# Kernel tuning notes

Measured on AMD Instinct MI355X. Metric: run time of the kernel, lower is better.

The kernel has to match this reference:

```python
import jax, jax.numpy as jnp
import numpy as np

N = 2048
D_MODEL = 1024
N_HEADS = 16
D_HEAD = D_MODEL // N_HEADS


def setup_inputs() -> dict:
    key = jax.random.key(0)
    ks = jax.random.split(key, 12)
    s = 1.0 / np.sqrt(D_MODEL)
    inp = {
        "x": jax.random.normal(ks[0], (N, D_MODEL), dtype=jnp.float32),
        "edge_bias": jax.random.normal(ks[1], (N, N, N_HEADS), dtype=jnp.float32) * 0.1,
        # torch.nn.Linear convention: y = x @ W.T + b, W: [out, in]
        "Wq": jax.random.normal(ks[2], (D_MODEL, D_MODEL), dtype=jnp.float32) * s,
        "bq": jax.random.normal(ks[3], (D_MODEL,), dtype=jnp.float32) * s,
        "Wk": jax.random.normal(ks[4], (D_MODEL, D_MODEL), dtype=jnp.float32) * s,
        "bk": jax.random.normal(ks[5], (D_MODEL,), dtype=jnp.float32) * s,
        "Wv": jax.random.normal(ks[6], (D_MODEL, D_MODEL), dtype=jnp.float32) * s,
        "bv": jax.random.normal(ks[7], (D_MODEL,), dtype=jnp.float32) * s,
        "Wo": jax.random.normal(ks[8], (D_MODEL, D_MODEL), dtype=jnp.float32) * s,
        "bo": jax.random.normal(ks[9], (D_MODEL,), dtype=jnp.float32) * s,
    }
    return inp


def reference(x, edge_bias, Wq, bq, Wk, bk, Wv, bv, Wo, bo):
    # x: [N, d], edge_bias: [N, N, H]
    scale = D_HEAD ** -0.5
    q = (x @ Wq.T + bq).reshape(N, N_HEADS, D_HEAD)  # [N, H, Dh]
    k = (x @ Wk.T + bk).reshape(N, N_HEADS, D_HEAD)
    v = (x @ Wv.T + bv).reshape(N, N_HEADS, D_HEAD)
    # attn[h, i, j] = q_i . k_j * scale + edge_bias[i, j, h]
    attn = jnp.einsum("nhd,mhd->hnm", q, k) * scale
    attn = attn + jnp.transpose(edge_bias, (2, 0, 1))
    attn = jax.nn.softmax(attn, axis=-1)
    # dropout is identity in eval/reference mode
    out = jnp.einsum("hnm,mhd->nhd", attn, v).reshape(N, D_MODEL)
    return out @ Wo.T + bo
```

## Files before the change

### kernel.cpp

```cpp
#include <hip/hip_runtime.h>
#include <math.h>

#define NTOK 2048
#define DM   1024
#define NH   16
#define DH   64
#define GM   2048
#define GN   1024
#define GK   1024
#define SCALE 0.125f

typedef __attribute__((ext_vector_type(8))) short short8;
typedef __attribute__((ext_vector_type(4))) float floatx4;
typedef unsigned short ushort_t;

__device__ __forceinline__ unsigned short f2bf(float f) {
    unsigned u = __builtin_bit_cast(unsigned, f);
    u += 0x7fffu + ((u >> 16) & 1u);
    return (unsigned short)(u >> 16);
}

__global__ __launch_bounds__(256) void convert5(
    const float* __restrict__ x,  const float* __restrict__ wq,
    const float* __restrict__ wk, const float* __restrict__ wv,
    const float* __restrict__ wo, ushort_t* __restrict__ dst)
{
    const size_t i4 = (size_t)blockIdx.x * 256 + threadIdx.x;
    const float* src; size_t off;
    if      (i4 <  524288) { src = x;  off = 0;       }
    else if (i4 <  786432) { src = wq; off = 524288;  }
    else if (i4 < 1048576) { src = wk; off = 786432;  }
    else if (i4 < 1310720) { src = wv; off = 1048576; }
    else                   { src = wo; off = 1310720; }
    float4 v = ((const float4*)src)[i4 - off];
    ushort4 o;
    o.x = f2bf(v.x); o.y = f2bf(v.y); o.z = f2bf(v.z); o.w = f2bf(v.w);
    ((ushort4*)dst)[i4] = o;
}

template<int BM, int BN>
__global__ __launch_bounds__(256) void gemm_bt(
    const ushort_t* __restrict__ A,
    const ushort_t* __restrict__ B0, const ushort_t* __restrict__ B1,
    const ushort_t* __restrict__ B2,
    const float* __restrict__ bi0, const float* __restrict__ bi1,
    const float* __restrict__ bi2,
    void* C0, void* C1, void* C2, int mode0, int mode1, int mode2)
{
    constexpr int AC = BM * 4 / 256;
    constexpr int BC = BN * 4 / 256;
    constexpr int FI = BM / 32;
    constexpr int FJ = BN / 32;
    constexpr int WM = BM / 2;
    constexpr int WN = BN / 2;

    const int z = blockIdx.z;
    const ushort_t* B   = (z == 0) ? B0  : (z == 1) ? B1  : B2;
    const float*    bia = (z == 0) ? bi0 : (z == 1) ? bi1 : bi2;
    void*           C   = (z == 0) ? C0  : (z == 1) ? C1  : C2;
    const int mode      = (z == 0) ? mode0 : (z == 1) ? mode1 : mode2;

    __shared__ __align__(16) ushort_t As[BM][32];
    __shared__ __align__(16) ushort_t Bs[BN][32];

    const int t    = threadIdx.x;
    const int w    = t >> 6;
    const int L    = t & 63;
    const int r16  = L & 15;
    const int quad = L >> 4;
    const int wm   = w & 1;
    const int wn   = w >> 1;

    const int m0 = blockIdx.y * BM;
    const int n0 = blockIdx.x * BN;

    const int srow = t >> 2;
    const int skc  = (t & 3) * 8;

    const ushort_t* ap = A + (size_t)(m0 + srow) * GK + skc;
    const ushort_t* bp = B + (size_t)(n0 + srow) * GK + skc;

    floatx4 acc[FI][FJ];
#pragma unroll
    for (int i = 0; i < FI; ++i)
#pragma unroll
        for (int j = 0; j < FJ; ++j) acc[i][j] = (floatx4){0.f, 0.f, 0.f, 0.f};

    short8 areg[AC], breg[BC];
#pragma unroll
    for (int c = 0; c < AC; ++c) areg[c] = *(const short8*)(ap + (size_t)c * 64 * GK);
#pragma unroll
    for (int c = 0; c < BC; ++c) breg[c] = *(const short8*)(bp + (size_t)c * 64 * GK);

    for (int ks = 0; ks < GK / 32; ++ks) {
        __syncthreads();
#pragma unroll
        for (int c = 0; c < AC; ++c) *(short8*)&As[c * 64 + srow][skc] = areg[c];
#pragma unroll
        for (int c = 0; c < BC; ++c) *(short8*)&Bs[c * 64 + srow][skc] = breg[c];
        __syncthreads();
        if (ks < GK / 32 - 1) {
            ap += 32; bp += 32;
#pragma unroll
            for (int c = 0; c < AC; ++c) areg[c] = *(const short8*)(ap + (size_t)c * 64 * GK);
#pragma unroll
            for (int c = 0; c < BC; ++c) breg[c] = *(const short8*)(bp + (size_t)c * 64 * GK);
        }
        short8 af[FI], bf[FJ];
#pragma unroll
        for (int fi = 0; fi < FI; ++fi)
            af[fi] = *(const short8*)&As[wm * WM + fi * 16 + r16][quad * 8];
#pragma unroll
        for (int fj = 0; fj < FJ; ++fj)
            bf[fj] = *(const short8*)&Bs[wn * WN + fj * 16 + r16][quad * 8];
#pragma unroll
        for (int fi = 0; fi < FI; ++fi)
#pragma unroll
            for (int fj = 0; fj < FJ; ++fj)
                acc[fi][fj] = __builtin_amdgcn_mfma_f32_16x16x32_bf16(
                    af[fi], bf[fj], acc[fi][fj], 0, 0, 0);
    }

#pragma unroll
    for (int fj = 0; fj < FJ; ++fj) {
        const int col = n0 + wn * WN + fj * 16 + r16;
        const float bv = bia[col];
#pragma unroll
        for (int fi = 0; fi < FI; ++fi) {
            const int row0 = m0 + wm * WM + fi * 16 + 4 * quad;
            floatx4 c = acc[fi][fj];
            if (mode == 2) {
                float* Cf = (float*)C;
#pragma unroll
                for (int i = 0; i < 4; ++i)
                    Cf[(size_t)(row0 + i) * GN + col] = c[i] + bv;
            } else if (mode == 0) {
                ushort_t* Cb = (ushort_t*)C;
#pragma unroll
                for (int i = 0; i < 4; ++i)
                    Cb[(size_t)(row0 + i) * GN + col] = f2bf(c[i] + bv);
            } else {
                ushort_t* Cb = (ushort_t*)C;
                ushort4 pk;
                pk.x = f2bf(c[0] + bv); pk.y = f2bf(c[1] + bv);
                pk.z = f2bf(c[2] + bv); pk.w = f2bf(c[3] + bv);
                *(ushort4*)(Cb + (size_t)col * GM + row0) = pk;
            }
        }
    }
}

#define NT (NTOK / 32)

__global__ __launch_bounds__(256) void attn2(
    const ushort_t* __restrict__ q, const ushort_t* __restrict__ k,
    const ushort_t* __restrict__ vT, const float* __restrict__ bias,
    ushort_t* __restrict__ ao)
{
    __shared__ float    Bb[2][4][16][33];
    __shared__ ushort_t Ps[4][16][40];

    const int b    = blockIdx.x;
    const int hg   = (b >> 3) & 3;
    const int it   = (b & 7) | ((b >> 5) << 3);
    const int i0   = it * 16;
    const int t    = threadIdx.x;
    const int w    = t >> 6;
    const int L    = t & 63;
    const int r16  = L & 15;
    const int quad = L >> 4;
    const int h    = hg * 4 + w;

#define kAddr(J0, JH, KC) (k  + (size_t)((J0) + (JH)*16 + r16) * DM + h*DH + (KC)*32 + quad*8)
#define vAddr(J0, DB)     (vT + (size_t)(h*DH + (DB)*16 + r16) * NTOK + (J0) + quad*8)
#define bAddr(J0, CI)     (bias + ((size_t)(i0 + (CI)*8 + (t>>5)) * NTOK + (J0) + (t&31)) * NH + hg*4)

    short8 qf[2];
#pragma unroll
    for (int kc = 0; kc < 2; ++kc)
        qf[kc] = *(const short8*)(q + (size_t)(i0 + r16) * DM + h * DH + kc * 32 + quad * 8);

    short8 kf[2][4];
    short8 vf[2][4];
    float4 bst[2];

    kf[0][0] = *(const short8*)kAddr(0, 0, 0);
    kf[0][1] = *(const short8*)kAddr(0, 0, 1);
    kf[0][2] = *(const short8*)kAddr(0, 1, 0);
    kf[0][3] = *(const short8*)kAddr(0, 1, 1);
    vf[0][0] = *(const short8*)vAddr(0, 0);
    vf[0][1] = *(const short8*)vAddr(0, 1);
    vf[0][2] = *(const short8*)vAddr(0, 2);
    vf[0][3] = *(const short8*)vAddr(0, 3);
    bst[0] = *(const float4*)bAddr(0, 0);
    bst[1] = *(const float4*)bAddr(0, 1);
    Bb[0][0][0 + (t >> 5)][t & 31] = bst[0].x;
    Bb[0][1][0 + (t >> 5)][t & 31] = bst[0].y;
    Bb[0][2][0 + (t >> 5)][t & 31] = bst[0].z;
    Bb[0][3][0 + (t >> 5)][t & 31] = bst[0].w;
    Bb[0][0][8 + (t >> 5)][t & 31] = bst[1].x;
    Bb[0][1][8 + (t >> 5)][t & 31] = bst[1].y;
    Bb[0][2][8 + (t >> 5)][t & 31] = bst[1].z;
    Bb[0][3][8 + (t >> 5)][t & 31] = bst[1].w;
    __syncthreads();

    floatx4 o[4];
#pragma unroll
    for (int d = 0; d < 4; ++d) o[d] = (floatx4){0.f, 0.f, 0.f, 0.f};
    float lrow[4] = {0.f, 0.f, 0.f, 0.f};

#define TILE(JT, CUR, NXT)                                                      \
  {                                                                             \
    const bool pre = (JT) < NT - 1;                                             \
    const int j0n = ((JT) + 1) * 32;                                            \
    if (pre) {                                                                  \
      kf[NXT][0] = *(const short8*)kAddr(j0n, 0, 0);                            \
      kf[NXT][1] = *(const short8*)kAddr(j0n, 0, 1);                            \
      kf[NXT][2] = *(const short8*)kAddr(j0n, 1, 0);                            \
      kf[NXT][3] = *(const short8*)kAddr(j0n, 1, 1);                            \
      vf[NXT][0] = *(const short8*)vAddr(j0n, 0);                               \
      vf[NXT][1] = *(const short8*)vAddr(j0n, 1);                               \
      vf[NXT][2] = *(const short8*)vAddr(j0n, 2);                               \
      vf[NXT][3] = *(const short8*)vAddr(j0n, 3);                               \
      bst[0] = *(const float4*)bAddr(j0n, 0);                                   \
      bst[1] = *(const float4*)bAddr(j0n, 1);                                   \
    }                                                                           \
    floatx4 s0 = (floatx4){0.f, 0.f, 0.f, 0.f};                                 \
    floatx4 s1 = (floatx4){0.f, 0.f, 0.f, 0.f};                                 \
    s0 = __builtin_amdgcn_mfma_f32_16x16x32_bf16(qf[0], kf[CUR][0], s0, 0,0,0); \
    s0 = __builtin_amdgcn_mfma_f32_16x16x32_bf16(qf[1], kf[CUR][1], s0, 0,0,0); \
    s1 = __builtin_amdgcn_mfma_f32_16x16x32_bf16(qf[0], kf[CUR][2], s1, 0,0,0); \
    s1 = __builtin_amdgcn_mfma_f32_16x16x32_bf16(qf[1], kf[CUR][3], s1, 0,0,0); \
    _Pragma("unroll")                                                           \
    for (int ii = 0; ii < 4; ++ii) {                                            \
      const float bv0 = Bb[CUR][w][4 * quad + ii][r16];                         \
      const float bv1 = Bb[CUR][w][4 * quad + ii][16 + r16];                    \
      const float p0 = __expf(fmaf(s0[ii], SCALE, bv0));                        \
      const float p1 = __expf(fmaf(s1[ii], SCALE, bv1));                        \
      lrow[ii] += p0 + p1;                                                      \
      Ps[w][4 * quad + ii][r16]      = f2bf(p0);                                \
      Ps[w][4 * quad + ii][16 + r16] = f2bf(p1);                                \
    }                                                                           \
    short8 pf = *(const short8*)&Ps[w][r16][quad * 8];                          \
    o[0] = __builtin_amdgcn_mfma_f32_16x16x32_bf16(pf, vf[CUR][0], o[0], 0,0,0);\
    o[1] = __builtin_amdgcn_mfma_f32_16x16x32_bf16(pf, vf[CUR][1], o[1], 0,0,0);\
    o[2] = __builtin_amdgcn_mfma_f32_16x16x32_bf16(pf, vf[CUR][2], o[2], 0,0,0);\
    o[3] = __builtin_amdgcn_mfma_f32_16x16x32_bf16(pf, vf[CUR][3], o[3], 0,0,0);\
    if (pre) {                                                                  \
      Bb[NXT][0][0 + (t >> 5)][t & 31] = bst[0].x;                              \
      Bb[NXT][1][0 + (t >> 5)][t & 31] = bst[0].y;                              \
      Bb[NXT][2][0 + (t >> 5)][t & 31] = bst[0].z;                              \
      Bb[NXT][3][0 + (t >> 5)][t & 31] = bst[0].w;                              \
      Bb[NXT][0][8 + (t >> 5)][t & 31] = bst[1].x;                              \
      Bb[NXT][1][8 + (t >> 5)][t & 31] = bst[1].y;                              \
      Bb[NXT][2][8 + (t >> 5)][t & 31] = bst[1].z;                              \
      Bb[NXT][3][8 + (t >> 5)][t & 31] = bst[1].w;                              \
    }                                                                           \
    __syncthreads();                                                            \
  }

    for (int jt = 0; jt < NT; jt += 2) {
        TILE(jt, 0, 1)
        TILE(jt + 1, 1, 0)
    }

    float inv[4];
#pragma unroll
    for (int ii = 0; ii < 4; ++ii) {
        float s = lrow[ii];
#pragma unroll
        for (int d = 1; d < 16; d <<= 1) s += __shfl_xor(s, d);
        inv[ii] = 1.f / s;
    }
#pragma unroll
    for (int db = 0; db < 4; ++db)
#pragma unroll
        for (int ii = 0; ii < 4; ++ii)
            ao[(size_t)(i0 + 4 * quad + ii) * DM + h * DH + db * 16 + r16] =
                f2bf(o[db][ii] * inv[ii]);
#undef TILE
#undef kAddr
#undef vAddr
#undef bAddr
}

extern "C" void kernel_launch(void* const* d_in, const int* in_sizes, int n_in,
                              void* d_out, int out_size, void* d_ws, size_t ws_size,
                              hipStream_t stream)
{
    const float* x  = (const float*)d_in[0];
    const float* eb = (const float*)d_in[1];
    const float* Wq = (const float*)d_in[2];
    const float* bq = (const float*)d_in[3];
    const float* Wk = (const float*)d_in[4];
    const float* bk = (const float*)d_in[5];
    const float* Wv = (const float*)d_in[6];
    const float* bv = (const float*)d_in[7];
    const float* Wo = (const float*)d_in[8];
    const float* bo = (const float*)d_in[9];
    float* out = (float*)d_out;
    (void)in_sizes; (void)n_in; (void)out_size; (void)ws_size;

    const size_t E1 = (size_t)1024 * 1024;
    ushort_t* wsb = (ushort_t*)d_ws;
    ushort_t* xb  = wsb;
    ushort_t* Wqb = wsb + 2 * E1;
    ushort_t* Wkb = wsb + 3 * E1;
    ushort_t* Wvb = wsb + 4 * E1;
    ushort_t* Wob = wsb + 5 * E1;
    ushort_t* qb  = wsb + 6 * E1;
    ushort_t* kb  = wsb + 8 * E1;
    ushort_t* vTb = wsb + 10 * E1;
    ushort_t* aob = wsb + 12 * E1;

    convert5<<<6144, 256, 0, stream>>>(x, Wq, Wk, Wv, Wo, wsb);

    {
        dim3 grid(GN / 64, GM / 128, 3);
        gemm_bt<128, 64><<<grid, 256, 0, stream>>>(
            xb, Wqb, Wkb, Wvb, bq, bk, bv,
            qb, kb, vTb, 0, 0, 1);
    }
    attn2<<<512, 256, 0, stream>>>(qb, kb, vTb, eb, aob);

    {
        dim3 grid(GN / 64, GM / 64, 1);
        gemm_bt<64, 64><<<grid, 256, 0, stream>>>(
            aob, Wob, Wob, Wob, bo, bo, bo,
            out, out, out, 2, 2, 2);
    }
}
```

Measured before the change: 530.3 us.

## Split attention key dimension into chunks with a separate partial-sum reduction kernel

The attention kernel now splits the key/value sequence into four chunks along a second grid dimension, raising the block count from 512 to 2048. Each block writes unnormalized fp32 partial outputs and per-row exp-sums to workspace. A new finalize kernel sums the partials, normalizes them and converts the result to bf16. The goal is better occupancy and latency hiding on a GPU with many CUs, at the cost of extra fp32 partial traffic, one more launch and more workspace.

```diff
diff --git a/kernel.cpp b/kernel.cpp
--- a/kernel.cpp
+++ b/kernel.cpp
@@ -150,17 +150,22 @@
     }
 }
 
-#define NT (NTOK / 32)
+#define NT   (NTOK / 32)
+#define NCH  4
+#define NTCH (NT / NCH)
+#define JCH  (NTOK / NCH)
 
 __global__ __launch_bounds__(256) void attn2(
     const ushort_t* __restrict__ q, const ushort_t* __restrict__ k,
     const ushort_t* __restrict__ vT, const float* __restrict__ bias,
-    ushort_t* __restrict__ ao)
+    float* __restrict__ opart, float* __restrict__ lpart)
 {
     __shared__ float    Bb[2][4][16][33];
     __shared__ ushort_t Ps[4][16][40];
 
     const int b    = blockIdx.x;
+    const int ch   = blockIdx.y;
+    const int jb   = ch * JCH;
     const int hg   = (b >> 3) & 3;
     const int it   = (b & 7) | ((b >> 5) << 3);
     const int i0   = it * 16;
@@ -184,16 +189,16 @@
     short8 vf[2][4];
     float4 bst[2];
 
-    kf[0][0] = *(const short8*)kAddr(0, 0, 0);
-    kf[0][1] = *(const short8*)kAddr(0, 0, 1);
-    kf[0][2] = *(const short8*)kAddr(0, 1, 0);
-    kf[0][3] = *(const short8*)kAddr(0, 1, 1);
-    vf[0][0] = *(const short8*)vAddr(0, 0);
-    vf[0][1] = *(const short8*)vAddr(0, 1);
-    vf[0][2] = *(const short8*)vAddr(0, 2);
-    vf[0][3] = *(const short8*)vAddr(0, 3);
-    bst[0] = *(const float4*)bAddr(0, 0);
-    bst[1] = *(const float4*)bAddr(0, 1);
+    kf[0][0] = *(const short8*)kAddr(jb, 0, 0);
+    kf[0][1] = *(const short8*)kAddr(jb, 0, 1);
+    kf[0][2] = *(const short8*)kAddr(jb, 1, 0);
+    kf[0][3] = *(const short8*)kAddr(jb, 1, 1);
+    vf[0][0] = *(const short8*)vAddr(jb, 0);
+    vf[0][1] = *(const short8*)vAddr(jb, 1);
+    vf[0][2] = *(const short8*)vAddr(jb, 2);
+    vf[0][3] = *(const short8*)vAddr(jb, 3);
+    bst[0] = *(const float4*)bAddr(jb, 0);
+    bst[1] = *(const float4*)bAddr(jb, 1);
     Bb[0][0][0 + (t >> 5)][t & 31] = bst[0].x;
     Bb[0][1][0 + (t >> 5)][t & 31] = bst[0].y;
     Bb[0][2][0 + (t >> 5)][t & 31] = bst[0].z;
@@ -211,8 +216,8 @@
 
 #define TILE(JT, CUR, NXT)                                                      \
   {                                                                             \
-    const bool pre = (JT) < NT - 1;                                             \
-    const int j0n = ((JT) + 1) * 32;                                            \
+    const bool pre = (JT) < NTCH - 1;                                           \
+    const int j0n = jb + ((JT) + 1) * 32;                                       \
     if (pre) {                                                                  \
       kf[NXT][0] = *(const short8*)kAddr(j0n, 0, 0);                            \
       kf[NXT][1] = *(const short8*)kAddr(j0n, 0, 1);                            \
@@ -259,29 +264,59 @@
     __syncthreads();                                                            \
   }
 
-    for (int jt = 0; jt < NT; jt += 2) {
+    for (int jt = 0; jt < NTCH; jt += 2) {
         TILE(jt, 0, 1)
         TILE(jt + 1, 1, 0)
     }
 
-    float inv[4];
+    float lred[4];
 #pragma unroll
     for (int ii = 0; ii < 4; ++ii) {
         float s = lrow[ii];
 #pragma unroll
         for (int d = 1; d < 16; d <<= 1) s += __shfl_xor(s, d);
-        inv[ii] = 1.f / s;
-    }
+        lred[ii] = s;
+    }
+    if (r16 == 0) {
+#pragma unroll
+        for (int ii = 0; ii < 4; ++ii)
+            lpart[(size_t)ch * NH * NTOK + (size_t)h * NTOK + i0 + 4 * quad + ii] = lred[ii];
+    }
+
+    float* op = opart + (size_t)ch * NTOK * DM;
 #pragma unroll
     for (int db = 0; db < 4; ++db)
 #pragma unroll
         for (int ii = 0; ii < 4; ++ii)
-            ao[(size_t)(i0 + 4 * quad + ii) * DM + h * DH + db * 16 + r16] =
-                f2bf(o[db][ii] * inv[ii]);
+            op[(size_t)(i0 + 4 * quad + ii) * DM + h * DH + db * 16 + r16] = o[db][ii];
 #undef TILE
 #undef kAddr
 #undef vAddr
 #undef bAddr
+}
+
+__global__ __launch_bounds__(256) void attn_fin(
+    const float* __restrict__ opart, const float* __restrict__ lpart,
+    ushort_t* __restrict__ ao)
+{
+    const int idx = blockIdx.x * 256 + threadIdx.x;
+    const int n   = idx >> 8;
+    const int d4  = idx & 255;
+    const int h   = d4 >> 4;
+    const size_t base = (size_t)n * DM + (size_t)d4 * 4;
+    float4 s = {0.f, 0.f, 0.f, 0.f};
+    float  l = 0.f;
+#pragma unroll
+    for (int c = 0; c < NCH; ++c) {
+        float4 p = *(const float4*)(opart + (size_t)c * NTOK * DM + base);
+        s.x += p.x; s.y += p.y; s.z += p.z; s.w += p.w;
+        l += lpart[(size_t)c * NH * NTOK + (size_t)h * NTOK + n];
+    }
+    const float inv = 1.f / l;
+    ushort4 o;
+    o.x = f2bf(s.x * inv); o.y = f2bf(s.y * inv);
+    o.z = f2bf(s.z * inv); o.w = f2bf(s.w * inv);
+    ((ushort4*)ao)[idx] = o;
 }
 
 extern "C" void kernel_launch(void* const* d_in, const int* in_sizes, int n_in,
@@ -312,6 +347,8 @@
     ushort_t* kb  = wsb + 8 * E1;
     ushort_t* vTb = wsb + 10 * E1;
     ushort_t* aob = wsb + 12 * E1;
+    float* opart = (float*)(wsb + 14 * E1);
+    float* lpart = opart + (size_t)NCH * NTOK * DM;
 
     convert5<<<6144, 256, 0, stream>>>(x, Wq, Wk, Wv, Wo, wsb);
 
@@ -321,7 +358,11 @@
             xb, Wqb, Wkb, Wvb, bq, bk, bv,
             qb, kb, vTb, 0, 0, 1);
     }
-    attn2<<<512, 256, 0, stream>>>(qb, kb, vTb, eb, aob);
+    {
+        dim3 grid(512, NCH, 1);
+        attn2<<<grid, 256, 0, stream>>>(qb, kb, vTb, eb, opart, lpart);
+    }
+    attn_fin<<<NTOK * DM / 4 / 256, 256, 0, stream>>>(opart, lpart, aob);
 
     {
         dim3 grid(GN / 64, GM / 64, 1);
```

After: 528.9 us. About the same (-0.3%).
